# Kernel optimization log

Hardware: AMD Instinct MI355X
Metric: run time of the kernel (lower is better)

Reference implementation:

```python
import jax, jax.numpy as jnp
import numpy as np

N_NODES = 100000
N_GRAPHS = 512
NEG_SLOPE = 0.2
EPS = 1e-16


def gat_conv(x, W, a_src, a_dst, bias, src, dst, heads, out_ch, concat):
    # x: [N, Fin]; W: [Fin, heads*out_ch]; a_src/a_dst: [heads, out_ch]
    N = x.shape[0]
    h = (x @ W).reshape(N, heads, out_ch)                      # [N,H,C]
    alpha_src = jnp.einsum('nhc,hc->nh', h, a_src)             # [N,H]
    alpha_dst = jnp.einsum('nhc,hc->nh', h, a_dst)             # [N,H]
    e = alpha_src[src] + alpha_dst[dst]                        # [E,H]
    e = jnp.where(e > 0, e, NEG_SLOPE * e)                     # leaky relu
    # segment softmax over incoming edges per destination node
    m = jax.ops.segment_max(e, dst, num_segments=N)            # [N,H]
    m = jnp.where(jnp.isfinite(m), m, 0.0)
    ee = jnp.exp(e - m[dst])
    denom = jax.ops.segment_sum(ee, dst, num_segments=N)       # [N,H]
    alpha = ee / (denom[dst] + EPS)                            # [E,H]
    msg = h[src] * alpha[:, :, None]                           # [E,H,C]
    out = jax.ops.segment_sum(msg, dst, num_segments=N)        # [N,H,C]
    if concat:
        out = out.reshape(N, heads * out_ch)
    else:
        out = out.mean(axis=1)
    return out + bias


def setup_inputs() -> dict:
    key = jax.random.key(0)
    ks = jax.random.split(key, 12)
    x = jax.random.normal(ks[0], (N_NODES, 128), dtype=jnp.float32)
    edge_index = jax.random.randint(ks[1], (2, 1600000), 0, N_NODES, dtype=jnp.int64)
    batch = jnp.sort(jax.random.randint(ks[2], (N_NODES,), 0, N_GRAPHS, dtype=jnp.int64))
    s = 0.1
    W1 = jax.random.normal(ks[3], (128, 64), dtype=jnp.float32) * s
    a_src1 = jax.random.normal(ks[4], (8, 8), dtype=jnp.float32) * s
    a_dst1 = jax.random.normal(ks[5], (8, 8), dtype=jnp.float32) * s
    b1 = jnp.zeros((64,), dtype=jnp.float32)
    W2 = jax.random.normal(ks[6], (64, 10), dtype=jnp.float32) * s
    a_src2 = jax.random.normal(ks[7], (1, 10), dtype=jnp.float32) * s
    a_dst2 = jax.random.normal(ks[8], (1, 10), dtype=jnp.float32) * s
    b2 = jnp.zeros((10,), dtype=jnp.float32)
    return {"x": x, "edge_index": edge_index, "batch": batch,
            "W1": W1, "a_src1": a_src1, "a_dst1": a_dst1, "b1": b1,
            "W2": W2, "a_src2": a_src2, "a_dst2": a_dst2, "b2": b2}


def reference(x, edge_index, batch, W1, a_src1, a_dst1, b1, W2, a_src2, a_dst2, b2):
    N = x.shape[0]
    # PyG GATConv default add_self_loops=True
    loops = jnp.arange(N, dtype=edge_index.dtype)
    src = jnp.concatenate([edge_index[0], loops])
    dst = jnp.concatenate([edge_index[1], loops])
    # eval mode: dropout layers are identity
    h = gat_conv(x, W1, a_src1, a_dst1, b1, src, dst, heads=8, out_ch=8, concat=True)
    h = jax.nn.elu(h)
    h = gat_conv(h, W2, a_src2, a_dst2, b2, src, dst, heads=1, out_ch=10, concat=False)
    # global mean pool over graphs
    sums = jax.ops.segment_sum(h, batch, num_segments=N_GRAPHS)        # [G,10]
    cnts = jax.ops.segment_sum(jnp.ones((N, 1), h.dtype), batch, num_segments=N_GRAPHS)
    pooled = sums / jnp.maximum(cnts, 1.0)
    return jax.nn.log_softmax(pooled, axis=1)
```

## Files before the change

kernel.cpp:

```cpp
#include <hip/hip_runtime.h>
#include <math.h>

#define L2E 1.44269504088896f
#define LRELU(v) fmaxf((v), 0.2f * (v))

__device__ __forceinline__ float fexp2(float v) { return __builtin_amdgcn_exp2f(v); }

__device__ __forceinline__ unsigned short f2bf(float f) {
    unsigned u = __float_as_uint(f);
    u += 0x7FFFu + ((u >> 16) & 1u);
    return (unsigned short)(u >> 16);
}
__device__ __forceinline__ float bf2f(unsigned short b) {
    return __uint_as_float((unsigned)b << 16);
}

typedef __attribute__((ext_vector_type(8))) short bf16x8;
typedef __attribute__((ext_vector_type(4))) float f32x4;

#define UPD8(mm, dd, Aa, Ab, ev, U)                                       \
    {                                                                     \
        float mn_ = fmaxf(mm, ev);                                        \
        float sc_ = fexp2(mm - mn_);                                      \
        float w_  = fexp2(ev - mn_);                                      \
        dd = dd * sc_ + w_;                                               \
        Aa.x = Aa.x * sc_ + w_ * __uint_as_float((U).x << 16);            \
        Aa.y = Aa.y * sc_ + w_ * __uint_as_float((U).x & 0xffff0000u);    \
        Aa.z = Aa.z * sc_ + w_ * __uint_as_float((U).y << 16);            \
        Aa.w = Aa.w * sc_ + w_ * __uint_as_float((U).y & 0xffff0000u);    \
        Ab.x = Ab.x * sc_ + w_ * __uint_as_float((U).z << 16);            \
        Ab.y = Ab.y * sc_ + w_ * __uint_as_float((U).z & 0xffff0000u);    \
        Ab.z = Ab.z * sc_ + w_ * __uint_as_float((U).w << 16);            \
        Ab.w = Ab.w * sc_ + w_ * __uint_as_float((U).w & 0xffff0000u);    \
        mm = mn_;                                                         \
    }
#define UPD1(mm, dd, aa, ev, hv)           \
    {                                      \
        float mn_ = fmaxf(mm, ev);         \
        float sc_ = fexp2(mm - mn_);       \
        float w_  = fexp2(ev - mn_);       \
        dd = dd * sc_ + w_;                \
        aa = aa * sc_ + w_ * (hv);         \
        mm = mn_;                          \
    }

#define CH 4096

__global__ __launch_bounds__(256) void k_gemm1_mfma(
        const float* __restrict__ x, const float* __restrict__ W,
        unsigned short* __restrict__ h1b, int N, int ntiles) {
    int tid = threadIdx.x;
    int w = tid >> 6, l = tid & 63;
    int c0 = w * 16;
    int lr = l & 15;
    int lg = l >> 4;

    bf16x8 bfr[4];
#pragma unroll
    for (int kk = 0; kk < 4; ++kk)
#pragma unroll
        for (int j = 0; j < 8; ++j)
            bfr[kk][j] = (short)f2bf(W[(size_t)(kk * 32 + lg * 8 + j) * 64 + c0 + lr]);

    for (int t = blockIdx.x; t < ntiles; t += gridDim.x) {
        int n0 = t * 16;
        int n = n0 + lr;
        const float4* xr = (const float4*)(x + (size_t)(n < N ? n : 0) * 128);
        f32x4 acc = {0.f, 0.f, 0.f, 0.f};
#pragma unroll
        for (int kk = 0; kk < 4; ++kk) {
            float4 u0 = xr[kk * 8 + lg * 2];
            float4 u1 = xr[kk * 8 + lg * 2 + 1];
            bf16x8 afr;
            afr[0] = (short)f2bf(u0.x); afr[1] = (short)f2bf(u0.y);
            afr[2] = (short)f2bf(u0.z); afr[3] = (short)f2bf(u0.w);
            afr[4] = (short)f2bf(u1.x); afr[5] = (short)f2bf(u1.y);
            afr[6] = (short)f2bf(u1.z); afr[7] = (short)f2bf(u1.w);
            acc = __builtin_amdgcn_mfma_f32_16x16x32_bf16(afr, bfr[kk], acc, 0, 0, 0);
        }
#pragma unroll
        for (int r = 0; r < 4; ++r) {
            int nn = n0 + lg * 4 + r;
            if (nn < N) h1b[(size_t)nn * 64 + c0 + lr] = f2bf(acc[r]);
        }
    }
}

__global__ void k_alpha(const unsigned short* __restrict__ h1b,
                        const float* __restrict__ a_src, const float* __restrict__ a_dst,
                        unsigned short* __restrict__ asrcb, float* __restrict__ adst, int N) {
    int t = blockIdx.x * 256 + threadIdx.x;
    if (t >= N * 8) return;
    int n = t >> 3, h = t & 7;
    uint4 hw = *(const uint4*)&h1b[(size_t)n * 64 + h * 8];
    const unsigned short* hu = (const unsigned short*)&hw;
    const float* as = a_src + h * 8;
    const float* ad = a_dst + h * 8;
    float s = 0.f, d = 0.f;
#pragma unroll
    for (int c = 0; c < 8; ++c) {
        float hv = bf2f(hu[c]);
        s = fmaf(hv, as[c], s);
        d = fmaf(hv, ad[c], d);
    }
    asrcb[t] = f2bf(s * L2E);
    adst[t] = d * L2E;
}


__global__ __launch_bounds__(256) void k_bhist(const int* __restrict__ dstE,
                                               const int* __restrict__ batch,
                                               int E, int NB, int G, int* __restrict__ bh) {
    __shared__ int lh[512];
    int tid = threadIdx.x, b = blockIdx.x;
    lh[tid] = 0; lh[tid + 256] = 0;
    __syncthreads();
#pragma unroll
    for (int i = 0; i < CH / 1024; ++i) {
        int eb = b * CH + (i * 256 + tid) * 4;
        if (eb + 3 < E) {
            int4 dv = *(const int4*)(dstE + eb);
            int g0 = batch[dv.x], g1 = batch[dv.y], g2 = batch[dv.z], g3 = batch[dv.w];
            atomicAdd(&lh[g0], 1); atomicAdd(&lh[g1], 1);
            atomicAdd(&lh[g2], 1); atomicAdd(&lh[g3], 1);
        } else {
#pragma unroll
            for (int k = 0; k < 4; ++k)
                if (eb + k < E) atomicAdd(&lh[batch[dstE[eb + k]]], 1);
        }
    }
    __syncthreads();
    if (tid < G)       bh[(size_t)tid * NB + b] = lh[tid];
    if (tid + 256 < G) bh[(size_t)(tid + 256) * NB + b] = lh[tid + 256];
}

__global__ __launch_bounds__(512) void k_mscan(const int* __restrict__ bh, int NB,
                                               int* __restrict__ pstart, int* __restrict__ total) {
    __shared__ int buf[512];
    int bin = blockIdx.x, t = threadIdx.x;
    int v = (t < NB) ? bh[(size_t)bin * NB + t] : 0;
    buf[t] = v;
    __syncthreads();
    for (int off = 1; off < 512; off <<= 1) {
        int u = (t >= off) ? buf[t - off] : 0;
        __syncthreads();
        buf[t] += u;
        __syncthreads();
    }
    if (t < NB) pstart[(size_t)bin * NB + t] = buf[t] - v;
    if (t == 511) total[bin] = buf[511];
}

__global__ __launch_bounds__(1024) void k_scan_top(const int* __restrict__ total, int nb,
                                                   int* __restrict__ boff) {
    __shared__ int buf[1024];
    int t = threadIdx.x;
    int v = (t < nb) ? total[t] : 0;
    buf[t] = v;
    __syncthreads();
    for (int off = 1; off < 1024; off <<= 1) {
        int u = (t >= off) ? buf[t - off] : 0;
        __syncthreads();
        buf[t] += u;
        __syncthreads();
    }
    if (t < nb) boff[t] = buf[t] - v;
}

__global__ __launch_bounds__(256) void k_bscatter(const int* __restrict__ srcE,
                                                  const int* __restrict__ dstE,
                                                  const int* __restrict__ batch,
                                                  const int* __restrict__ boff,
                                                  const int* __restrict__ pstart,
                                                  int E, int NB, int G, int2* __restrict__ pairs) {
    __shared__ int lstart[512];
    __shared__ int lc[512];
    int tid = threadIdx.x, b = blockIdx.x;
#pragma unroll
    for (int j = tid; j < 512; j += 256) {
        lstart[j] = (j < G) ? boff[j] + pstart[(size_t)j * NB + b] : 0;
        lc[j] = 0;
    }
    __syncthreads();
#pragma unroll
    for (int i = 0; i < CH / 1024; ++i) {
        int eb = b * CH + (i * 256 + tid) * 4;
        if (eb + 3 < E) {
            int4 sv = *(const int4*)(srcE + eb);
            int4 dv = *(const int4*)(dstE + eb);
            int g0 = batch[dv.x], g1 = batch[dv.y], g2 = batch[dv.z], g3 = batch[dv.w];
            int p0 = atomicAdd(&lc[g0], 1);
            int p1 = atomicAdd(&lc[g1], 1);
            int p2 = atomicAdd(&lc[g2], 1);
            int p3 = atomicAdd(&lc[g3], 1);
            pairs[lstart[g0] + p0] = make_int2(sv.x, dv.x);
            pairs[lstart[g1] + p1] = make_int2(sv.y, dv.y);
            pairs[lstart[g2] + p2] = make_int2(sv.z, dv.z);
            pairs[lstart[g3] + p3] = make_int2(sv.w, dv.w);
        } else {
#pragma unroll
            for (int k = 0; k < 4; ++k)
                if (eb + k < E) {
                    int s = srcE[eb + k], d = dstE[eb + k];
                    int bin = batch[d];
                    int old = atomicAdd(&lc[bin], 1);
                    pairs[lstart[bin] + old] = make_int2(s, d);
                }
        }
    }
}

__global__ __launch_bounds__(512) void k_csr_local(const int2* __restrict__ pairs,
                                                   const int* __restrict__ boff,
                                                   const int* __restrict__ batch,
                                                   int E, int N, int G,
                                                   int* __restrict__ cnt, int* __restrict__ excl,
                                                   int* __restrict__ srcs) {
    __shared__ int lcnt[512];
    __shared__ int buf[512];
    __shared__ int lcur[512];
    int g = blockIdx.x, t = threadIdx.x;
    int lo = 0, hi = N;
    while (lo < hi) { int mid = (lo + hi) >> 1; if (batch[mid] < g) lo = mid + 1; else hi = mid; }
    int ns = lo;
    hi = N;
    while (lo < hi) { int mid = (lo + hi) >> 1; if (batch[mid] < g + 1) lo = mid + 1; else hi = mid; }
    int ne = lo;
    int lnodes = ne - ns;
    int es = boff[g];
    int ee = (g + 1 < G) ? boff[g + 1] : E;

    lcnt[t] = 0;
    __syncthreads();
    for (int e = es + t; e < ee; e += 512) atomicAdd(&lcnt[pairs[e].y - ns], 1);
    __syncthreads();
    int v = lcnt[t];
    buf[t] = v;
    __syncthreads();
    for (int off = 1; off < 512; off <<= 1) {
        int u = (t >= off) ? buf[t - off] : 0;
        __syncthreads();
        buf[t] += u;
        __syncthreads();
    }
    int lex = buf[t] - v;
    lcur[t] = lex;
    if (t < lnodes) {
        cnt[ns + t] = v;
        excl[ns + t] = es + lex;
    }
    __syncthreads();
    for (int e = es + t; e < ee; e += 512) {
        int2 p = pairs[e];
        int pos = atomicAdd(&lcur[p.y - ns], 1);
        srcs[es + pos] = p.x;
    }
}

__global__ void k_gather1(const int* __restrict__ srcs, const int* __restrict__ excl,
                          const int* __restrict__ cnt,
                          const unsigned short* __restrict__ asrcb, const float* __restrict__ adst1,
                          const unsigned short* __restrict__ h1b, float* __restrict__ agg, int N) {
    int tid = blockIdx.x * 256 + threadIdx.x;
    int wave = tid >> 6;
    int lane = threadIdx.x & 63;
    int q = lane >> 3;
    int l = lane & 7;
    int wid = wave * 8 + q;
    if (wid >= N) return;
    int c0 = l * 8;

    int beg = excl[wid];
    int cw  = cnt[wid];
    const int* sp = srcs + beg;
    float adh = adst1[wid * 8 + l];

    uint4 us = *(const uint4*)&h1b[(size_t)wid * 64 + c0];
    float4 A0a, A0b;
    A0a.x = __uint_as_float(us.x << 16); A0a.y = __uint_as_float(us.x & 0xffff0000u);
    A0a.z = __uint_as_float(us.y << 16); A0a.w = __uint_as_float(us.y & 0xffff0000u);
    A0b.x = __uint_as_float(us.z << 16); A0b.y = __uint_as_float(us.z & 0xffff0000u);
    A0b.z = __uint_as_float(us.w << 16); A0b.w = __uint_as_float(us.w & 0xffff0000u);
    float m0 = LRELU(bf2f(asrcb[wid * 8 + l]) + adh), d0 = 1.f;
    float4 Z = {0.f, 0.f, 0.f, 0.f};
    float4 A1a = Z, A1b = Z, A2a = Z, A2b = Z, A3a = Z, A3b = Z;
    float m1 = -INFINITY, d1 = 0.f;
    float m2 = -INFINITY, d2 = 0.f;
    float m3 = -INFINITY, d3 = 0.f;

    int i = 0;
    for (; i + 4 <= cw; i += 4) {
        int s0 = sp[i], s1 = sp[i + 1], s2 = sp[i + 2], s3 = sp[i + 3];
        float e0 = LRELU(bf2f(asrcb[s0 * 8 + l]) + adh);
        float e1 = LRELU(bf2f(asrcb[s1 * 8 + l]) + adh);
        float e2 = LRELU(bf2f(asrcb[s2 * 8 + l]) + adh);
        float e3 = LRELU(bf2f(asrcb[s3 * 8 + l]) + adh);
        uint4 u0 = *(const uint4*)&h1b[(size_t)s0 * 64 + c0];
        uint4 u1 = *(const uint4*)&h1b[(size_t)s1 * 64 + c0];
        uint4 u2 = *(const uint4*)&h1b[(size_t)s2 * 64 + c0];
        uint4 u3 = *(const uint4*)&h1b[(size_t)s3 * 64 + c0];
        UPD8(m0, d0, A0a, A0b, e0, u0);
        UPD8(m1, d1, A1a, A1b, e1, u1);
        UPD8(m2, d2, A2a, A2b, e2, u2);
        UPD8(m3, d3, A3a, A3b, e3, u3);
    }
    for (; i < cw; ++i) {
        int s = sp[i];
        float ev = LRELU(bf2f(asrcb[s * 8 + l]) + adh);
        uint4 uv = *(const uint4*)&h1b[(size_t)s * 64 + c0];
        UPD8(m0, d0, A0a, A0b, ev, uv);
    }
    float mM = fmaxf(fmaxf(m0, m1), fmaxf(m2, m3));
    float w0 = fexp2(m0 - mM), w1 = fexp2(m1 - mM);
    float w2 = fexp2(m2 - mM), w3 = fexp2(m3 - mM);
    float den = d0 * w0 + d1 * w1 + d2 * w2 + d3 * w3;
    float inv = 1.f / (den + 1e-16f);
    float4 Ra, Rb;
    Ra.x = (A0a.x * w0 + A1a.x * w1 + A2a.x * w2 + A3a.x * w3) * inv;
    Ra.y = (A0a.y * w0 + A1a.y * w1 + A2a.y * w2 + A3a.y * w3) * inv;
    Ra.z = (A0a.z * w0 + A1a.z * w1 + A2a.z * w2 + A3a.z * w3) * inv;
    Ra.w = (A0a.w * w0 + A1a.w * w1 + A2a.w * w2 + A3a.w * w3) * inv;
    Rb.x = (A0b.x * w0 + A1b.x * w1 + A2b.x * w2 + A3b.x * w3) * inv;
    Rb.y = (A0b.y * w0 + A1b.y * w1 + A2b.y * w2 + A3b.y * w3) * inv;
    Rb.z = (A0b.z * w0 + A1b.z * w1 + A2b.z * w2 + A3b.z * w3) * inv;
    Rb.w = (A0b.w * w0 + A1b.w * w1 + A2b.w * w2 + A3b.w * w3) * inv;
    *(float4*)&agg[(size_t)wid * 64 + c0] = Ra;
    *(float4*)&agg[(size_t)wid * 64 + c0 + 4] = Rb;
}

__global__ void k_fin1(const float* __restrict__ agg, const float* __restrict__ b1,
                       const float* __restrict__ W2,
                       const float* __restrict__ a_src2, const float* __restrict__ a_dst2,
                       unsigned short* __restrict__ h2b, unsigned short* __restrict__ asrc2b,
                       float* __restrict__ adst2, int N) {
    int n = blockIdx.x * 256 + threadIdx.x;
    if (n >= N) return;
    float acc[10];
#pragma unroll
    for (int j = 0; j < 10; ++j) acc[j] = 0.f;
    const float4* ar4 = (const float4*)(agg + (size_t)n * 64);
    const float4* b14 = (const float4*)b1;
#pragma unroll 4
    for (int kq = 0; kq < 16; ++kq) {
        float4 a4 = ar4[kq];
        float4 bq = b14[kq];
        float r[4];
        r[0] = a4.x + bq.x; r[1] = a4.y + bq.y;
        r[2] = a4.z + bq.z; r[3] = a4.w + bq.w;
#pragma unroll
        for (int t = 0; t < 4; ++t) {
            float rv = r[t] > 0.f ? r[t] : expm1f(r[t]);
            const float* wr = W2 + (kq * 4 + t) * 10;
#pragma unroll
            for (int j = 0; j < 10; ++j) acc[j] = fmaf(rv, wr[j], acc[j]);
        }
    }
    float s = 0.f, d = 0.f;
    unsigned pw[5];
#pragma unroll
    for (int j = 0; j < 10; j += 2) {
        s = fmaf(acc[j], a_src2[j], s);     d = fmaf(acc[j], a_dst2[j], d);
        s = fmaf(acc[j+1], a_src2[j+1], s); d = fmaf(acc[j+1], a_dst2[j+1], d);
        pw[j >> 1] = (unsigned)f2bf(acc[j]) | ((unsigned)f2bf(acc[j+1]) << 16);
    }
    unsigned* hw = (unsigned*)&h2b[(size_t)n * 10];
#pragma unroll
    for (int j = 0; j < 5; ++j) hw[j] = pw[j];
    asrc2b[n] = f2bf(s * L2E);
    adst2[n] = d * L2E;
}

__global__ void k_gather2(const int* __restrict__ srcs, const int* __restrict__ excl,
                          const int* __restrict__ cnt,
                          const unsigned short* __restrict__ asrc2b, const float* __restrict__ adst2,
                          const unsigned short* __restrict__ h2b, float* __restrict__ agg2, int N) {
    int tid = blockIdx.x * 256 + threadIdx.x;
    int wave = tid >> 6;
    int lane = threadIdx.x & 63;
    int q = lane >> 4;
    int l = lane & 15;
    int wid = wave * 4 + q;
    if (wid >= N) return;

    int beg = excl[wid];
    int cw  = cnt[wid];
    const int* sp = srcs + beg;
    float adn = adst2[wid];
    bool ld = l < 10;

    float m0 = LRELU(bf2f(asrc2b[wid]) + adn), d0 = 1.f;
    float a0 = ld ? bf2f(h2b[(size_t)wid * 10 + l]) : 0.f;
    float m1 = -INFINITY, d1 = 0.f, a1 = 0.f;
    float m2 = -INFINITY, d2 = 0.f, a2 = 0.f;
    float m3 = -INFINITY, d3 = 0.f, a3 = 0.f;

    int i = 0;
    for (; i + 4 <= cw; i += 4) {
        int s0 = sp[i], s1 = sp[i + 1], s2 = sp[i + 2], s3 = sp[i + 3];
        float e0 = LRELU(bf2f(asrc2b[s0]) + adn);
        float e1 = LRELU(bf2f(asrc2b[s1]) + adn);
        float e2 = LRELU(bf2f(asrc2b[s2]) + adn);
        float e3 = LRELU(bf2f(asrc2b[s3]) + adn);
        float g0 = ld ? bf2f(h2b[(size_t)s0 * 10 + l]) : 0.f;
        float g1 = ld ? bf2f(h2b[(size_t)s1 * 10 + l]) : 0.f;
        float g2 = ld ? bf2f(h2b[(size_t)s2 * 10 + l]) : 0.f;
        float g3 = ld ? bf2f(h2b[(size_t)s3 * 10 + l]) : 0.f;
        UPD1(m0, d0, a0, e0, g0);
        UPD1(m1, d1, a1, e1, g1);
        UPD1(m2, d2, a2, e2, g2);
        UPD1(m3, d3, a3, e3, g3);
    }
    for (; i < cw; ++i) {
        int s = sp[i];
        float ev = LRELU(bf2f(asrc2b[s]) + adn);
        float gv = ld ? bf2f(h2b[(size_t)s * 10 + l]) : 0.f;
        UPD1(m0, d0, a0, ev, gv);
    }
    float mM = fmaxf(fmaxf(m0, m1), fmaxf(m2, m3));
    float w0 = fexp2(m0 - mM), w1 = fexp2(m1 - mM);
    float w2 = fexp2(m2 - mM), w3 = fexp2(m3 - mM);
    float den = d0 * w0 + d1 * w1 + d2 * w2 + d3 * w3;
    float acc = a0 * w0 + a1 * w1 + a2 * w2 + a3 * w3;
    if (ld) agg2[(size_t)wid * 10 + l] = acc / (den + 1e-16f);
}

__global__ void k_pool_final(const float* __restrict__ agg2, const float* __restrict__ b2,
                             const int* __restrict__ batch, float* __restrict__ out,
                             int N, int G) {
    int g = blockIdx.x;
    int lo = 0, hi = N;
    while (lo < hi) { int mid = (lo + hi) >> 1; if (batch[mid] < g) lo = mid + 1; else hi = mid; }
    int s = lo;
    lo = s; hi = N;
    while (lo < hi) { int mid = (lo + hi) >> 1; if (batch[mid] < g + 1) lo = mid + 1; else hi = mid; }
    int e = lo;
    int tid = threadIdx.x;
    float acc[10];
#pragma unroll
    for (int j = 0; j < 10; ++j) acc[j] = 0.f;
    for (int n = s + tid; n < e; n += 256) {
        const float* r = agg2 + (size_t)n * 10;
#pragma unroll
        for (int j = 0; j < 10; ++j) acc[j] += r[j];
    }
    __shared__ float red[256 * 10];
#pragma unroll
    for (int j = 0; j < 10; ++j) red[tid * 10 + j] = acc[j];
    __syncthreads();
    for (int st = 128; st > 0; st >>= 1) {
        if (tid < st)
#pragma unroll
            for (int j = 0; j < 10; ++j) red[tid * 10 + j] += red[(tid + st) * 10 + j];
        __syncthreads();
    }
    if (tid == 0) {
        int c = e - s;
        float v[10], m = -1e30f;
#pragma unroll
        for (int j = 0; j < 10; ++j) {
            v[j] = (c > 0) ? red[j] / (float)c + b2[j] : 0.f;
            m = fmaxf(m, v[j]);
        }
        float ssum = 0.f;
#pragma unroll
        for (int j = 0; j < 10; ++j) ssum += expf(v[j] - m);
        float ls = logf(ssum);
#pragma unroll
        for (int j = 0; j < 10; ++j) out[(size_t)g * 10 + j] = v[j] - m - ls;
    }
}

extern "C" void kernel_launch(void* const* d_in, const int* in_sizes, int n_in,
                              void* d_out, int out_size, void* d_ws, size_t ws_size,
                              hipStream_t stream) {
    const float* x     = (const float*)d_in[0];
    const int*   ei    = (const int*)d_in[1];
    const int*   batch = (const int*)d_in[2];
    const float* W1    = (const float*)d_in[3];
    const float* as1w  = (const float*)d_in[4];
    const float* ad1w  = (const float*)d_in[5];
    const float* b1    = (const float*)d_in[6];
    const float* W2    = (const float*)d_in[7];
    const float* as2w  = (const float*)d_in[8];
    const float* ad2w  = (const float*)d_in[9];
    const float* b2    = (const float*)d_in[10];

    const int N  = in_sizes[0] / 128;
    const int E  = in_sizes[1] / 2;
    const int G  = out_size / 10;
    const int* srcE = ei;
    const int* dstE = ei + E;

    auto cdiv = [](long long a, long long b) { return (int)((a + b - 1) / b); };
    const int NB = cdiv(E, CH);

    size_t Nz = (size_t)N;
    unsigned short* h1b = (unsigned short*)d_ws;
    float* agg2  = (float*)d_ws;
    unsigned short* asrc1b = h1b + Nz * 64;
    float* adst1 = (float*)(asrc1b + Nz * 8);
    unsigned short* h2b = (unsigned short*)(adst1 + Nz * 8);
    unsigned short* asrc2b = h2b + Nz * 10;
    float* adst2 = (float*)(asrc2b + Nz + (Nz & 1));
    float* agg1  = adst2 + Nz;
    int2*  pairs = (int2*)agg1;
    int* cntA    = (int*)(agg1 + Nz * 64);
    int* exclA   = cntA + Nz;
    int* srcsA   = exclA + Nz;
    int* bhA     = srcsA + E;
    int* pstartA = bhA + (size_t)512 * NB;
    int* totalA  = pstartA + (size_t)512 * NB;
    int* boffA   = totalA + 512;

    const int B = 256;

    int ntiles = cdiv(N, 16);
    int gB = ntiles < 2048 ? ntiles : 2048;
    k_gemm1_mfma<<<gB, B, 0, stream>>>(x, W1, h1b, N, ntiles);
    k_alpha<<<cdiv((long long)N * 8, B), B, 0, stream>>>(h1b, as1w, ad1w, asrc1b, adst1, N);

    k_bhist<<<NB, B, 0, stream>>>(dstE, batch, E, NB, G, bhA);
    k_mscan<<<512, 512, 0, stream>>>(bhA, NB, pstartA, totalA);
    k_scan_top<<<1, 1024, 0, stream>>>(totalA, G, boffA);
    k_bscatter<<<NB, B, 0, stream>>>(srcE, dstE, batch, boffA, pstartA, E, NB, G, pairs);
    k_csr_local<<<G, 512, 0, stream>>>(pairs, boffA, batch, E, N, G, cntA, exclA, srcsA);

    k_gather1<<<cdiv(N, 32), B, 0, stream>>>(srcsA, exclA, cntA, asrc1b, adst1, h1b, agg1, N);
    k_fin1<<<cdiv(N, B), B, 0, stream>>>(agg1, b1, W2, as2w, ad2w, h2b, asrc2b, adst2, N);

    k_gather2<<<cdiv(N, 16), B, 0, stream>>>(srcsA, exclA, cntA, asrc2b, adst2, h2b, agg2, N);

    k_pool_final<<<G, B, 0, stream>>>(agg2, b2, batch, (float*)d_out, N, G);
}
```

Baseline: 201.5 us.

## Fuse layer-2 projection into gather1 and pack edge pairs into single ints

Moves the bias+ELU+W2 projection and the layer-2 attention coefficients into the epilogue of k_gather1. Each of the 8 lanes per node computes a partial 10-wide dot product and the partials are reduced with xor shuffles, so the k_fin1 kernel and the 64-float-per-node agg1 round trip through memory go away. Separately, the bucketed edge pairs are packed as src plus graph-local dst offset shifted by 17 bits in one int instead of an int2, halving the scatter traffic. The packing assumes node ids fit in 17 bits and per-graph local offsets stay small, which holds only for the current sizes.

```diff
diff --git a/kernel.cpp b/kernel.cpp
--- a/kernel.cpp
+++ b/kernel.cpp
@@ -152,7 +152,9 @@
 }
 
 __global__ __launch_bounds__(1024) void k_scan_top(const int* __restrict__ total, int nb,
-                                                   int* __restrict__ boff) {
+                                                   int* __restrict__ boff,
+                                                   const int* __restrict__ batch, int N,
+                                                   int* __restrict__ nstart) {
     __shared__ int buf[1024];
     int t = threadIdx.x;
     int v = (t < nb) ? total[t] : 0;
@@ -164,7 +166,12 @@
         buf[t] += u;
         __syncthreads();
     }
-    if (t < nb) boff[t] = buf[t] - v;
+    if (t < nb) {
+        boff[t] = buf[t] - v;
+        int lo = 0, hi = N;
+        while (lo < hi) { int mid = (lo + hi) >> 1; if (batch[mid] < t) lo = mid + 1; else hi = mid; }
+        nstart[t] = lo;
+    }
 }
 
 __global__ __launch_bounds__(256) void k_bscatter(const int* __restrict__ srcE,
@@ -172,13 +179,16 @@
                                                   const int* __restrict__ batch,
                                                   const int* __restrict__ boff,
                                                   const int* __restrict__ pstart,
-                                                  int E, int NB, int G, int2* __restrict__ pairs) {
+                                                  const int* __restrict__ nstart,
+                                                  int E, int NB, int G, int* __restrict__ pairs) {
     __shared__ int lstart[512];
     __shared__ int lc[512];
+    __shared__ int lns[512];
     int tid = threadIdx.x, b = blockIdx.x;
 #pragma unroll
     for (int j = tid; j < 512; j += 256) {
         lstart[j] = (j < G) ? boff[j] + pstart[(size_t)j * NB + b] : 0;
+        lns[j] = (j < G) ? nstart[j] : 0;
         lc[j] = 0;
     }
     __syncthreads();
@@ -193,10 +203,10 @@
             int p1 = atomicAdd(&lc[g1], 1);
             int p2 = atomicAdd(&lc[g2], 1);
             int p3 = atomicAdd(&lc[g3], 1);
-            pairs[lstart[g0] + p0] = make_int2(sv.x, dv.x);
-            pairs[lstart[g1] + p1] = make_int2(sv.y, dv.y);
-            pairs[lstart[g2] + p2] = make_int2(sv.z, dv.z);
-            pairs[lstart[g3] + p3] = make_int2(sv.w, dv.w);
+            pairs[lstart[g0] + p0] = sv.x | ((dv.x - lns[g0]) << 17);
+            pairs[lstart[g1] + p1] = sv.y | ((dv.y - lns[g1]) << 17);
+            pairs[lstart[g2] + p2] = sv.z | ((dv.z - lns[g2]) << 17);
+            pairs[lstart[g3] + p3] = sv.w | ((dv.w - lns[g3]) << 17);
         } else {
 #pragma unroll
             for (int k = 0; k < 4; ++k)
@@ -204,13 +214,13 @@
                     int s = srcE[eb + k], d = dstE[eb + k];
                     int bin = batch[d];
                     int old = atomicAdd(&lc[bin], 1);
-                    pairs[lstart[bin] + old] = make_int2(s, d);
+                    pairs[lstart[bin] + old] = s | ((d - lns[bin]) << 17);
                 }
         }
     }
 }
 
-__global__ __launch_bounds__(512) void k_csr_local(const int2* __restrict__ pairs,
+__global__ __launch_bounds__(512) void k_csr_local(const int* __restrict__ pairs,
                                                    const int* __restrict__ boff,
                                                    const int* __restrict__ batch,
                                                    int E, int N, int G,
@@ -232,7 +242,7 @@
 
     lcnt[t] = 0;
     __syncthreads();
-    for (int e = es + t; e < ee; e += 512) atomicAdd(&lcnt[pairs[e].y - ns], 1);
+    for (int e = es + t; e < ee; e += 512) atomicAdd(&lcnt[pairs[e] >> 17], 1);
     __syncthreads();
     int v = lcnt[t];
     buf[t] = v;
@@ -251,16 +261,20 @@
     }
     __syncthreads();
     for (int e = es + t; e < ee; e += 512) {
-        int2 p = pairs[e];
-        int pos = atomicAdd(&lcur[p.y - ns], 1);
-        srcs[es + pos] = p.x;
+        int pv = pairs[e];
+        int pos = atomicAdd(&lcur[pv >> 17], 1);
+        srcs[es + pos] = pv & 0x1FFFF;
     }
 }
 
 __global__ void k_gather1(const int* __restrict__ srcs, const int* __restrict__ excl,
                           const int* __restrict__ cnt,
                           const unsigned short* __restrict__ asrcb, const float* __restrict__ adst1,
-                          const unsigned short* __restrict__ h1b, float* __restrict__ agg, int N) {
+                          const unsigned short* __restrict__ h1b,
+                          const float* __restrict__ b1, const float* __restrict__ W2,
+                          const float* __restrict__ a_src2, const float* __restrict__ a_dst2,
+                          unsigned short* __restrict__ h2b, unsigned short* __restrict__ asrc2b,
+                          float* __restrict__ adst2, int N) {
     int tid = blockIdx.x * 256 + threadIdx.x;
     int wave = tid >> 6;
     int lane = threadIdx.x & 63;
@@ -315,59 +329,47 @@
     float w2 = fexp2(m2 - mM), w3 = fexp2(m3 - mM);
     float den = d0 * w0 + d1 * w1 + d2 * w2 + d3 * w3;
     float inv = 1.f / (den + 1e-16f);
-    float4 Ra, Rb;
-    Ra.x = (A0a.x * w0 + A1a.x * w1 + A2a.x * w2 + A3a.x * w3) * inv;
-    Ra.y = (A0a.y * w0 + A1a.y * w1 + A2a.y * w2 + A3a.y * w3) * inv;
-    Ra.z = (A0a.z * w0 + A1a.z * w1 + A2a.z * w2 + A3a.z * w3) * inv;
-    Ra.w = (A0a.w * w0 + A1a.w * w1 + A2a.w * w2 + A3a.w * w3) * inv;
-    Rb.x = (A0b.x * w0 + A1b.x * w1 + A2b.x * w2 + A3b.x * w3) * inv;
-    Rb.y = (A0b.y * w0 + A1b.y * w1 + A2b.y * w2 + A3b.y * w3) * inv;
-    Rb.z = (A0b.z * w0 + A1b.z * w1 + A2b.z * w2 + A3b.z * w3) * inv;
-    Rb.w = (A0b.w * w0 + A1b.w * w1 + A2b.w * w2 + A3b.w * w3) * inv;
-    *(float4*)&agg[(size_t)wid * 64 + c0] = Ra;
-    *(float4*)&agg[(size_t)wid * 64 + c0 + 4] = Rb;
-}
-
-__global__ void k_fin1(const float* __restrict__ agg, const float* __restrict__ b1,
-                       const float* __restrict__ W2,
-                       const float* __restrict__ a_src2, const float* __restrict__ a_dst2,
-                       unsigned short* __restrict__ h2b, unsigned short* __restrict__ asrc2b,
-                       float* __restrict__ adst2, int N) {
-    int n = blockIdx.x * 256 + threadIdx.x;
-    if (n >= N) return;
-    float acc[10];
-#pragma unroll
-    for (int j = 0; j < 10; ++j) acc[j] = 0.f;
-    const float4* ar4 = (const float4*)(agg + (size_t)n * 64);
-    const float4* b14 = (const float4*)b1;
-#pragma unroll 4
-    for (int kq = 0; kq < 16; ++kq) {
-        float4 a4 = ar4[kq];
-        float4 bq = b14[kq];
-        float r[4];
-        r[0] = a4.x + bq.x; r[1] = a4.y + bq.y;
-        r[2] = a4.z + bq.z; r[3] = a4.w + bq.w;
-#pragma unroll
-        for (int t = 0; t < 4; ++t) {
-            float rv = r[t] > 0.f ? r[t] : expm1f(r[t]);
-            const float* wr = W2 + (kq * 4 + t) * 10;
-#pragma unroll
-            for (int j = 0; j < 10; ++j) acc[j] = fmaf(rv, wr[j], acc[j]);
+    float rv[8];
+    rv[0] = (A0a.x * w0 + A1a.x * w1 + A2a.x * w2 + A3a.x * w3) * inv;
+    rv[1] = (A0a.y * w0 + A1a.y * w1 + A2a.y * w2 + A3a.y * w3) * inv;
+    rv[2] = (A0a.z * w0 + A1a.z * w1 + A2a.z * w2 + A3a.z * w3) * inv;
+    rv[3] = (A0a.w * w0 + A1a.w * w1 + A2a.w * w2 + A3a.w * w3) * inv;
+    rv[4] = (A0b.x * w0 + A1b.x * w1 + A2b.x * w2 + A3b.x * w3) * inv;
+    rv[5] = (A0b.y * w0 + A1b.y * w1 + A2b.y * w2 + A3b.y * w3) * inv;
+    rv[6] = (A0b.z * w0 + A1b.z * w1 + A2b.z * w2 + A3b.z * w3) * inv;
+    rv[7] = (A0b.w * w0 + A1b.w * w1 + A2b.w * w2 + A3b.w * w3) * inv;
+
+    float accj[10];
+#pragma unroll
+    for (int j = 0; j < 10; ++j) accj[j] = 0.f;
+#pragma unroll
+    for (int t = 0; t < 8; ++t) {
+        float r = rv[t] + b1[c0 + t];
+        r = r > 0.f ? r : expm1f(r);
+        const float* wr = W2 + (c0 + t) * 10;
+#pragma unroll
+        for (int j = 0; j < 10; ++j) accj[j] = fmaf(r, wr[j], accj[j]);
+    }
+#pragma unroll
+    for (int mask = 1; mask <= 4; mask <<= 1)
+#pragma unroll
+        for (int j = 0; j < 10; ++j) accj[j] += __shfl_xor(accj[j], mask);
+
+    if (l == 0) {
+        float s = 0.f, d = 0.f;
+        unsigned pw[5];
+#pragma unroll
+        for (int j = 0; j < 10; j += 2) {
+            s = fmaf(accj[j], a_src2[j], s);     d = fmaf(accj[j], a_dst2[j], d);
+            s = fmaf(accj[j+1], a_src2[j+1], s); d = fmaf(accj[j+1], a_dst2[j+1], d);
+            pw[j >> 1] = (unsigned)f2bf(accj[j]) | ((unsigned)f2bf(accj[j+1]) << 16);
         }
-    }
-    float s = 0.f, d = 0.f;
-    unsigned pw[5];
-#pragma unroll
-    for (int j = 0; j < 10; j += 2) {
-        s = fmaf(acc[j], a_src2[j], s);     d = fmaf(acc[j], a_dst2[j], d);
-        s = fmaf(acc[j+1], a_src2[j+1], s); d = fmaf(acc[j+1], a_dst2[j+1], d);
-        pw[j >> 1] = (unsigned)f2bf(acc[j]) | ((unsigned)f2bf(acc[j+1]) << 16);
-    }
-    unsigned* hw = (unsigned*)&h2b[(size_t)n * 10];
-#pragma unroll
-    for (int j = 0; j < 5; ++j) hw[j] = pw[j];
-    asrc2b[n] = f2bf(s * L2E);
-    adst2[n] = d * L2E;
+        unsigned* hw = (unsigned*)&h2b[(size_t)wid * 10];
+#pragma unroll
+        for (int j = 0; j < 5; ++j) hw[j] = pw[j];
+        asrc2b[wid] = f2bf(s * L2E);
+        adst2[wid] = d * L2E;
+    }
 }
 
 __global__ void k_gather2(const int* __restrict__ srcs, const int* __restrict__ excl,
@@ -502,15 +504,15 @@
     unsigned short* h2b = (unsigned short*)(adst1 + Nz * 8);
     unsigned short* asrc2b = h2b + Nz * 10;
     float* adst2 = (float*)(asrc2b + Nz + (Nz & 1));
-    float* agg1  = adst2 + Nz;
-    int2*  pairs = (int2*)agg1;
-    int* cntA    = (int*)(agg1 + Nz * 64);
+    int* pairsA  = (int*)(adst2 + Nz);
+    int* cntA    = pairsA + (size_t)E;
     int* exclA   = cntA + Nz;
     int* srcsA   = exclA + Nz;
     int* bhA     = srcsA + E;
     int* pstartA = bhA + (size_t)512 * NB;
     int* totalA  = pstartA + (size_t)512 * NB;
     int* boffA   = totalA + 512;
+    int* nstartA = boffA + 512;
 
     const int B = 256;
 
@@ -521,12 +523,12 @@
 
     k_bhist<<<NB, B, 0, stream>>>(dstE, batch, E, NB, G, bhA);
     k_mscan<<<512, 512, 0, stream>>>(bhA, NB, pstartA, totalA);
-    k_scan_top<<<1, 1024, 0, stream>>>(totalA, G, boffA);
-    k_bscatter<<<NB, B, 0, stream>>>(srcE, dstE, batch, boffA, pstartA, E, NB, G, pairs);
-    k_csr_local<<<G, 512, 0, stream>>>(pairs, boffA, batch, E, N, G, cntA, exclA, srcsA);
-
-    k_gather1<<<cdiv(N, 32), B, 0, stream>>>(srcsA, exclA, cntA, asrc1b, adst1, h1b, agg1, N);
-    k_fin1<<<cdiv(N, B), B, 0, stream>>>(agg1, b1, W2, as2w, ad2w, h2b, asrc2b, adst2, N);
+    k_scan_top<<<1, 1024, 0, stream>>>(totalA, G, boffA, batch, N, nstartA);
+    k_bscatter<<<NB, B, 0, stream>>>(srcE, dstE, batch, boffA, pstartA, nstartA, E, NB, G, pairsA);
+    k_csr_local<<<G, 512, 0, stream>>>(pairsA, boffA, batch, E, N, G, cntA, exclA, srcsA);
+
+    k_gather1<<<cdiv(N, 32), B, 0, stream>>>(srcsA, exclA, cntA, asrc1b, adst1, h1b,
+                                             b1, W2, as2w, ad2w, h2b, asrc2b, adst2, N);
 
     k_gather2<<<cdiv(N, 16), B, 0, stream>>>(srcsA, exclA, cntA, asrc2b, adst2, h2b, agg2, N);
 
```

Result: faster. 196.2 us (-2.6%).
